# Kernel tuning notes

Measured on AMD Instinct MI355X. Metric: run time of the kernel, lower is better.

The kernel has to match this reference:

```python
import jax, jax.numpy as jnp
import numpy as np

N, T, D, H = 256, 128, 512, 1024


def setup_inputs() -> dict:
    key = jax.random.key(0)
    k_x, k_A, k_Wx, k_Wh, k_Wa = jax.random.split(key, 5)
    x = jax.random.normal(k_x, (N, T, D), dtype=jnp.float32)
    A = jax.random.normal(k_A, (N, H, 4, 4), dtype=jnp.float32)
    Wx = jax.random.normal(k_Wx, (D, 4 * H), dtype=jnp.float32) / np.sqrt(D)
    Wh = jax.random.normal(k_Wh, (H, 4 * H), dtype=jnp.float32) / np.sqrt(H)
    Wattn = jax.random.normal(k_Wa, (H, 4 * H), dtype=jnp.float32) / np.sqrt(H)
    b = jnp.zeros((4 * H,), dtype=jnp.float32)
    return {"x": x, "A": A, "Wx": Wx, "Wh": Wh, "Wattn": Wattn, "b": b}


def _attention_lstm(x, A, Wx, Wh, Wattn, b):
    # A: (N, H, 4, 4) -> flatten spatial to (N, H, 16)
    A_flat = A.reshape(A.shape[0], A.shape[1], -1)
    h0 = A_flat.mean(axis=2)  # (N, H)
    c0 = h0
    Hdim = h0.shape[1]
    scale = 1.0 / jnp.sqrt(jnp.asarray(Hdim, dtype=x.dtype))

    def step(carry, x_t):
        prev_h, prev_c = carry
        # scaled dot-product attention over 16 spatial locations
        scores = jnp.einsum("nh,nhs->ns", prev_h, A_flat) * scale  # (N, 16)
        w = jax.nn.softmax(scores, axis=1)
        attn = jnp.einsum("nhs,ns->nh", A_flat, w)  # (N, H)
        # fused LSTM gates
        a = x_t @ Wx + prev_h @ Wh + attn @ Wattn + b  # (N, 4H)
        i = jax.nn.sigmoid(a[:, 0:Hdim])
        f = jax.nn.sigmoid(a[:, Hdim:2 * Hdim])
        o = jax.nn.sigmoid(a[:, 2 * Hdim:3 * Hdim])
        g = jnp.tanh(a[:, 3 * Hdim:4 * Hdim])
        next_c = f * prev_c + i * g
        next_h = o * jnp.tanh(next_c)
        return (next_h, next_c), next_h

    x_tnd = jnp.swapaxes(x, 0, 1)  # (T, N, D)
    _, h_tnh = jax.lax.scan(step, (h0, c0), x_tnd)
    return jnp.swapaxes(h_tnh, 0, 1)  # (N, T, H)


def reference(x, A, Wx, Wh, Wattn, b):
    return _attention_lstm(x, A, Wx, Wh, Wattn, b)
```

## Files before the change

### kernel.cpp

```cpp
#include <hip/hip_runtime.h>
#include <math.h>

#define NB 256
#define TT 128
#define DD 512
#define HH 1024
#define KHX 1536
#define KFB 2560
#define BK 128
#define NBLK2 256
#define NCHUNK 24

typedef _Float16 half_t;
typedef _Float16 half8 __attribute__((ext_vector_type(8)));
typedef _Float16 half4v __attribute__((ext_vector_type(4)));
typedef float f32x4 __attribute__((ext_vector_type(4)));


__global__ __launch_bounds__(256) void k_trans(const float* __restrict__ src,
        half_t* __restrict__ dst, int kstride, int koff, int nkt) {
    __shared__ half_t tile[64][65];
    int bk = blockIdx.x % nkt;
    int bn = blockIdx.x / nkt;
    int k0 = bk * 64, n0 = bn * 64;
    #pragma unroll
    for (int i = 0; i < 16; ++i) {
        int idx = i * 256 + threadIdx.x;
        int r = idx >> 6, c = idx & 63;
        tile[c][r] = (half_t)src[(size_t)(k0 + r) * 4096 + n0 + c];
    }
    __syncthreads();
    #pragma unroll
    for (int i = 0; i < 16; ++i) {
        int idx = i * 256 + threadIdx.x;
        int r = idx >> 6, c = idx & 63;
        dst[(size_t)(n0 + r) * kstride + koff + k0 + c] = tile[r][c];
    }
}

__global__ __launch_bounds__(256) void k_convX(const float* __restrict__ x,
        half_t* __restrict__ x16) {
    size_t base = ((size_t)blockIdx.x * 256 + threadIdx.x) * 32;
    #pragma unroll
    for (int u = 0; u < 4; ++u) {
        float4 a = ((const float4*)(x + base))[2 * u];
        float4 c = ((const float4*)(x + base))[2 * u + 1];
        half8 p;
        p[0] = (half_t)a.x; p[1] = (half_t)a.y; p[2] = (half_t)a.z; p[3] = (half_t)a.w;
        p[4] = (half_t)c.x; p[5] = (half_t)c.y; p[6] = (half_t)c.z; p[7] = (half_t)c.w;
        ((half8*)(x16 + base))[u] = p;
    }
}

__global__ __launch_bounds__(256) void k_convA(const float* __restrict__ A,
        half_t* __restrict__ A16, half_t* __restrict__ AsT,
        float* __restrict__ cbuf, half_t* __restrict__ h16,
        float* __restrict__ sc0, float* __restrict__ sc1, float* __restrict__ sc2) {
    __shared__ float sred[4][16];
    int n = blockIdx.x, tid = threadIdx.x;
    float ps[16];
    #pragma unroll
    for (int s = 0; s < 16; ++s) ps[s] = 0.f;
    #pragma unroll
    for (int r = 0; r < 4; ++r) {
        int h = tid + r * 256;
        const float4* ap = (const float4*)(A + ((size_t)n * HH + h) * 16);
        float4 v0 = ap[0], v1 = ap[1], v2 = ap[2], v3 = ap[3];
        float a[16];
        a[0]=v0.x; a[1]=v0.y; a[2] =v0.z; a[3] =v0.w;
        a[4]=v1.x; a[5]=v1.y; a[6] =v1.z; a[7] =v1.w;
        a[8]=v2.x; a[9]=v2.y; a[10]=v2.z; a[11]=v2.w;
        a[12]=v3.x; a[13]=v3.y; a[14]=v3.z; a[15]=v3.w;
        float hv = 0.f;
        #pragma unroll
        for (int s = 0; s < 16; ++s) hv += a[s];
        hv *= (1.f / 16.f);
        size_t ci = (size_t)n * HH + h;
        cbuf[ci] = hv;
        h16[ci] = (half_t)hv;
        half8 q0, q1;
        #pragma unroll
        for (int s = 0; s < 8; ++s) { q0[s] = (half_t)a[s]; q1[s] = (half_t)a[s + 8]; }
        *(half8*)(A16 + ci * 16) = q0;
        *(half8*)(A16 + ci * 16 + 8) = q1;
        #pragma unroll
        for (int s = 0; s < 16; ++s)
            AsT[(size_t)n * 16 * HH + (size_t)s * HH + h] = (half_t)a[s];
        #pragma unroll
        for (int s = 0; s < 16; ++s) ps[s] += hv * a[s];
    }
    #pragma unroll
    for (int off = 32; off; off >>= 1)
        #pragma unroll
        for (int s = 0; s < 16; ++s) ps[s] += __shfl_xor(ps[s], off, 64);
    int wave = tid >> 6;
    if ((tid & 63) == 0)
        #pragma unroll
        for (int s = 0; s < 16; ++s) sred[wave][s] = ps[s];
    __syncthreads();
    if (tid < 16) {
        sc0[n * 16 + tid] = sred[0][tid] + sred[1][tid] + sred[2][tid] + sred[3][tid];
        sc1[n * 16 + tid] = 0.f;
        sc2[n * 16 + tid] = 0.f;
    }
}

__global__ __launch_bounds__(256) void k_gemm_G(const half_t* __restrict__ AsT,
        const half_t* __restrict__ WaT, half_t* __restrict__ G16) {
    __shared__ half_t sAs[16][BK + 8];
    __shared__ half_t sB[4][16][BK + 8];
    int bid = blockIdx.x;
    int n = bid >> 6, jt = bid & 63;
    int j0 = jt * 16;
    int tid = threadIdx.x, wv = tid >> 6, lane = tid & 63;
    f32x4 acc = {};
    int srB = tid >> 2, scB = (tid & 3) * 32;
    int gB = srB >> 4, jcB = srB & 15;
    for (int it = 0; it < HH / BK; ++it) {
        int k0 = it * BK;
        if (tid < 128) {
            int r = tid >> 3, c = (tid & 7) * 16;
            const uint4* sp = (const uint4*)(AsT + (size_t)n * 16 * HH + (size_t)r * HH + k0 + c);
            uint4 u0 = sp[0], u1 = sp[1];
            *(uint4*)&sAs[r][c] = u0;
            *(uint4*)&sAs[r][c + 8] = u1;
        }
        {
            const half_t* src = WaT + ((size_t)(gB * HH + j0 + jcB)) * HH + k0 + scB;
            uint4 u0 = ((const uint4*)src)[0];
            uint4 u1 = ((const uint4*)src)[1];
            uint4 u2 = ((const uint4*)src)[2];
            uint4 u3 = ((const uint4*)src)[3];
            *((uint4*)&sB[gB][jcB][scB])      = u0;
            *((uint4*)&sB[gB][jcB][scB + 8])  = u1;
            *((uint4*)&sB[gB][jcB][scB + 16]) = u2;
            *((uint4*)&sB[gB][jcB][scB + 24]) = u3;
        }
        __syncthreads();
        int row16 = lane & 15, kg = lane >> 4;
        #pragma unroll
        for (int kc = 0; kc < BK / 32; ++kc) {
            half8 bf = *(const half8*)&sB[wv][row16][kc * 32 + kg * 8];
            half8 af = *(const half8*)&sAs[row16][kc * 32 + kg * 8];
            acc = __builtin_amdgcn_mfma_f32_16x16x32_f16(af, bf, acc, 0, 0, 0);
        }
        __syncthreads();
    }
    int col = lane & 15, rbase = (lane >> 4) * 4;
    size_t jf = (size_t)wv * HH + j0 + col;
    half4v o;
    o[0] = (half_t)acc[0]; o[1] = (half_t)acc[1];
    o[2] = (half_t)acc[2]; o[3] = (half_t)acc[3];
    *(half4v*)(G16 + ((size_t)n * 4096 + jf) * 16 + rbase) = o;
}


struct StepLds {
    half_t W[32][1544];
    union {
        half_t H[2][128][72];
        struct {
            float pe[128][33];
            char  _pad[18432 - sizeof(float) * 128 * 33];
            float ps[128][20];
        } e;
    } u;
};

__device__ __forceinline__ void grid_sync2(int* cnt, volatile int* flag, int inst) {
    __syncthreads();
    if (threadIdx.x == 0) {
        __threadfence();
        int prev = __hip_atomic_fetch_add(cnt, 1, __ATOMIC_ACQ_REL,
                                          __HIP_MEMORY_SCOPE_AGENT);
        if (prev == NBLK2 * (inst + 1) - 1) {
            __hip_atomic_store((int*)flag, inst + 1, __ATOMIC_RELEASE,
                               __HIP_MEMORY_SCOPE_AGENT);
        } else {
            int guard = 0;
            while (__hip_atomic_load((int*)flag, __ATOMIC_RELAXED,
                                     __HIP_MEMORY_SCOPE_AGENT) < inst + 1) {
                __builtin_amdgcn_s_sleep(2);
                if (++guard > (1 << 24)) break;
            }
        }
        __threadfence();
    }
    __syncthreads();
}

__global__ __launch_bounds__(256, 1) void k_steps2(
        const half_t* __restrict__ x16, half_t* __restrict__ h16A,
        half_t* __restrict__ h16B, const half_t* __restrict__ WhxT,
        const half_t* __restrict__ A16, const half_t* __restrict__ G16,
        const float* __restrict__ b, const float* __restrict__ cbuf,
        float* __restrict__ sc0, float* __restrict__ sc1, float* __restrict__ sc2,
        float* __restrict__ out, int* __restrict__ bar) {
    __shared__ StepLds L;
    int bid = blockIdx.x;
    int mhalf = bid & 1;
    int jb = bid >> 1;
    int n0 = mhalf * 128;
    int tid = threadIdx.x, wv = tid >> 6, lane = tid & 63;
    int la = lane & 15, kg = lane >> 4;
    int srow = tid & 127, shalf = tid >> 7;
    int* cnt = bar;
    volatile int* flag = (volatile int*)(bar + 32);

    {
        int wr = tid >> 3;
        int seg = tid & 7;
        int g = wr >> 3, jj = wr & 7;
        const half_t* wsrc = WhxT + (size_t)(g * HH + jb * 8 + jj) * KHX + seg * 192;
        #pragma unroll
        for (int i = 0; i < 24; ++i) {
            uint4 u = ((const uint4*)wsrc)[i];
            *(uint4*)&L.W[wr][seg * 192 + i * 8] = u;
        }
    }

    int n_l = tid & 127;
    int u4 = (tid >> 7) * 4;
    int n = n0 + n_l;
    int jbase = jb * 8 + u4;
    half8 gq[4][8];
    #pragma unroll
    for (int g = 0; g < 4; ++g) {
        const half8* gsrc = (const half8*)(G16 + ((size_t)n * 4096 + g * HH + jbase) * 16);
        #pragma unroll
        for (int i = 0; i < 8; ++i) gq[g][i] = gsrc[i];
    }
    half8 aq[8];
    {
        const half8* asrc = (const half8*)(A16 + ((size_t)n * HH + jbase) * 16);
        #pragma unroll
        for (int i = 0; i < 8; ++i) aq[i] = asrc[i];
    }
    float bb[4][4];
    #pragma unroll
    for (int g = 0; g < 4; ++g) {
        float4 bv = *(const float4*)(b + g * HH + jbase);
        bb[g][0] = bv.x; bb[g][1] = bv.y; bb[g][2] = bv.z; bb[g][3] = bv.w;
    }
    float creg[4];
    {
        float4 cv = *(const float4*)(cbuf + (size_t)n * HH + jbase);
        creg[0] = cv.x; creg[1] = cv.y; creg[2] = cv.z; creg[3] = cv.w;
    }

    float* scC = sc0; float* scN = sc1; float* scZ = sc2;
    half_t* h16c = h16A; half_t* h16n = h16B;

    uint4 pA0, pA1, pA2, pA3, pB0, pB1, pB2, pB3;

#define STAGE_SRC(c) ((c) < 8 \
    ? x16 + ((size_t)(n0 + srow) * TT + t) * DD + (c) * 64 + shalf * 32 \
    : h16c + (size_t)(n0 + srow) * HH + ((c) - 8) * 64 + shalf * 32)
#define STAGE_LOAD_A(c) { const uint4* sp_ = (const uint4*)STAGE_SRC(c); \
    pA0 = sp_[0]; pA1 = sp_[1]; pA2 = sp_[2]; pA3 = sp_[3]; }
#define STAGE_LOAD_B(c) { const uint4* sp_ = (const uint4*)STAGE_SRC(c); \
    pB0 = sp_[0]; pB1 = sp_[1]; pB2 = sp_[2]; pB3 = sp_[3]; }
#define STAGE_WRITE_A(BUF) { \
    *(uint4*)&L.u.H[BUF][srow][shalf * 32 + 0]  = pA0; \
    *(uint4*)&L.u.H[BUF][srow][shalf * 32 + 8]  = pA1; \
    *(uint4*)&L.u.H[BUF][srow][shalf * 32 + 16] = pA2; \
    *(uint4*)&L.u.H[BUF][srow][shalf * 32 + 24] = pA3; }
#define STAGE_WRITE_B(BUF) { \
    *(uint4*)&L.u.H[BUF][srow][shalf * 32 + 0]  = pB0; \
    *(uint4*)&L.u.H[BUF][srow][shalf * 32 + 8]  = pB1; \
    *(uint4*)&L.u.H[BUF][srow][shalf * 32 + 16] = pB2; \
    *(uint4*)&L.u.H[BUF][srow][shalf * 32 + 24] = pB3; }
#define COMPUTE(BUF, c) { \
    _Pragma("unroll") \
    for (int ks = 0; ks < 2; ++ks) { \
        half8 a0 = *(const half8*)&L.u.H[BUF][wv * 32 + la][ks * 32 + kg * 8]; \
        half8 a1 = *(const half8*)&L.u.H[BUF][wv * 32 + 16 + la][ks * 32 + kg * 8]; \
        half8 b0 = *(const half8*)&L.W[la][(c) * 64 + ks * 32 + kg * 8]; \
        half8 b1 = *(const half8*)&L.W[16 + la][(c) * 64 + ks * 32 + kg * 8]; \
        acc00 = __builtin_amdgcn_mfma_f32_16x16x32_f16(a0, b0, acc00, 0, 0, 0); \
        acc01 = __builtin_amdgcn_mfma_f32_16x16x32_f16(a0, b1, acc01, 0, 0, 0); \
        acc10 = __builtin_amdgcn_mfma_f32_16x16x32_f16(a1, b0, acc10, 0, 0, 0); \
        acc11 = __builtin_amdgcn_mfma_f32_16x16x32_f16(a1, b1, acc11, 0, 0, 0); \
    } }

    for (int t = 0; t < TT; ++t) {
        float w16[16];
        {
            const float4* sp = (const float4*)(scC + (size_t)n * 16);
            float4 q0 = sp[0], q1 = sp[1], q2 = sp[2], q3 = sp[3];
            float sc[16] = {q0.x, q0.y, q0.z, q0.w, q1.x, q1.y, q1.z, q1.w,
                            q2.x, q2.y, q2.z, q2.w, q3.x, q3.y, q3.z, q3.w};
            float m = -1e30f;
            #pragma unroll
            for (int s = 0; s < 16; ++s) { sc[s] *= 0.03125f; m = fmaxf(m, sc[s]); }
            float den = 0.f;
            #pragma unroll
            for (int s = 0; s < 16; ++s) { sc[s] = expf(sc[s] - m); den += sc[s]; }
            float inv = 1.f / den;
            #pragma unroll
            for (int s = 0; s < 16; ++s) w16[s] = sc[s] * inv;
        }
        if (bid < 16) scZ[bid * 256 + tid] = 0.f;

        f32x4 acc00 = {}, acc01 = {}, acc10 = {}, acc11 = {};
        STAGE_LOAD_A(0); STAGE_WRITE_A(0); STAGE_LOAD_B(1);
        __syncthreads();
        for (int d = 0; d < 12; ++d) {
            int c0 = 2 * d, c1 = 2 * d + 1;
            COMPUTE(0, c0);
            STAGE_WRITE_B(1);
            if (c0 + 2 < NCHUNK) STAGE_LOAD_A(c0 + 2);
            __syncthreads();
            COMPUTE(1, c1);
            if (c0 + 2 < NCHUNK) STAGE_WRITE_A(0);
            if (c1 + 2 < NCHUNK) STAGE_LOAD_B(c1 + 2);
            __syncthreads();
        }

        {
            int rbase = kg * 4;
            #pragma unroll
            for (int q = 0; q < 4; ++q) {
                L.u.e.pe[wv * 32 + rbase + q][la]           = acc00[q];
                L.u.e.pe[wv * 32 + rbase + q][16 + la]      = acc01[q];
                L.u.e.pe[wv * 32 + 16 + rbase + q][la]      = acc10[q];
                L.u.e.pe[wv * 32 + 16 + rbase + q][16 + la] = acc11[q];
            }
        }
        __syncthreads();

        float v[4][4];
        #pragma unroll
        for (int g = 0; g < 4; ++g)
            #pragma unroll
            for (int j = 0; j < 4; ++j)
                v[g][j] = L.u.e.pe[n_l][g * 8 + u4 + j] + bb[g][j];
        #pragma unroll
        for (int g = 0; g < 4; ++g)
            #pragma unroll
            for (int j = 0; j < 4; ++j) {
                float a0 = 0.f;
                #pragma unroll
                for (int s = 0; s < 16; ++s)
                    a0 += w16[s] * (float)gq[g][j * 2 + (s >> 3)][s & 7];
                v[g][j] += a0;
            }
        float hv[4];
        #pragma unroll
        for (int j = 0; j < 4; ++j) {
            float ig = 1.f / (1.f + expf(-v[0][j]));
            float fg = 1.f / (1.f + expf(-v[1][j]));
            float og = 1.f / (1.f + expf(-v[2][j]));
            float gg = tanhf(v[3][j]);
            float cn = fg * creg[j] + ig * gg;
            creg[j] = cn;
            hv[j] = og * tanhf(cn);
        }
        {
            float4 o4; o4.x = hv[0]; o4.y = hv[1]; o4.z = hv[2]; o4.w = hv[3];
            *(float4*)(out + ((size_t)n * TT + t) * HH + jbase) = o4;
            half4v h4; h4[0] = (half_t)hv[0]; h4[1] = (half_t)hv[1];
            h4[2] = (half_t)hv[2]; h4[3] = (half_t)hv[3];
            *(half4v*)(h16n + (size_t)n * HH + jbase) = h4;
        }
        float p[16];
        #pragma unroll
        for (int s = 0; s < 16; ++s) {
            float a0 = hv[0] * (float)aq[0 * 2 + (s >> 3)][s & 7]
                     + hv[1] * (float)aq[1 * 2 + (s >> 3)][s & 7]
                     + hv[2] * (float)aq[2 * 2 + (s >> 3)][s & 7]
                     + hv[3] * (float)aq[3 * 2 + (s >> 3)][s & 7];
            p[s] = a0;
        }
        if (tid < 128) {
            #pragma unroll
            for (int s = 0; s < 16; ++s) L.u.e.ps[n_l][s] = p[s];
        }
        __syncthreads();
        if (tid >= 128) {
            #pragma unroll
            for (int s = 0; s < 16; ++s) L.u.e.ps[n_l][s] += p[s];
        }
        __syncthreads();
        {
            int sh = (tid >> 7) * 8;
            #pragma unroll
            for (int i = 0; i < 8; ++i)
                atomicAdd(scN + (size_t)n * 16 + sh + i, L.u.e.ps[n_l][sh + i]);
        }

        if (t + 1 < TT) grid_sync2(cnt, flag, t);
        float* tmp = scC; scC = scN; scN = scZ; scZ = tmp;
        half_t* th = h16c; h16c = h16n; h16n = th;
    }
#undef STAGE_SRC
#undef STAGE_LOAD_A
#undef STAGE_LOAD_B
#undef STAGE_WRITE_A
#undef STAGE_WRITE_B
#undef COMPUTE
}


union LdsS {
    struct {
        half_t sA[32][BK + 8];
        half_t sB[4][16][BK + 8];
    } s;
    float pe[4][32][16];
};

__global__ __launch_bounds__(256) void k_step(const float* __restrict__ x,
        const half_t* __restrict__ h16c, half_t* __restrict__ h16n,
        const half_t* __restrict__ WhxT, const half_t* __restrict__ A16,
        const half_t* __restrict__ G16, const float* __restrict__ b,
        float* __restrict__ cbuf, const float* __restrict__ scC,
        float* __restrict__ scN, float* __restrict__ scZ,
        float* __restrict__ out, int t) {
    __shared__ LdsS L;
    __shared__ float wlds[32][16];
    int bid = blockIdx.x;
    int xcd = bid & 7, slot = bid >> 3;
    int mtile = slot & 7, jtile = slot >> 3;
    int n0 = mtile * 32;
    int j0 = xcd * 128 + jtile * 16;
    int tid = threadIdx.x, wv = tid >> 6, lane = tid & 63;

    if (bid < 16) scZ[bid * 256 + tid] = 0.f;
    if (tid < 32) {
        int n = n0 + tid;
        const float4* sp = (const float4*)(scC + n * 16);
        float4 u0 = sp[0], u1 = sp[1], u2 = sp[2], u3 = sp[3];
        float sc[16] = {u0.x, u0.y, u0.z, u0.w, u1.x, u1.y, u1.z, u1.w,
                        u2.x, u2.y, u2.z, u2.w, u3.x, u3.y, u3.z, u3.w};
        float m = -1e30f;
        #pragma unroll
        for (int s = 0; s < 16; ++s) { sc[s] *= 0.03125f; m = fmaxf(m, sc[s]); }
        float den = 0.f;
        #pragma unroll
        for (int s = 0; s < 16; ++s) { sc[s] = expf(sc[s] - m); den += sc[s]; }
        float inv = 1.f / den;
        #pragma unroll
        for (int s = 0; s < 16; ++s) wlds[tid][s] = sc[s] * inv;
    }

    f32x4 acc[2] = {};
    int srA = tid >> 3, scA = (tid & 7) * 16;
    int srB = tid >> 2, scB = (tid & 3) * 32;
    int gB = srB >> 4, jcB = srB & 15;

    for (int it = 0; it < KHX / BK; ++it) {
        int k0 = it * BK;
        {
            int n = n0 + srA;
            if (k0 < DD) {
                const float* src = x + ((size_t)n * TT + t) * DD + k0 + scA;
                float4 v0 = ((const float4*)src)[0];
                float4 v1 = ((const float4*)src)[1];
                float4 v2 = ((const float4*)src)[2];
                float4 v3 = ((const float4*)src)[3];
                half8 p0, p1;
                p0[0] = (half_t)v0.x; p0[1] = (half_t)v0.y; p0[2] = (half_t)v0.z; p0[3] = (half_t)v0.w;
                p0[4] = (half_t)v1.x; p0[5] = (half_t)v1.y; p0[6] = (half_t)v1.z; p0[7] = (half_t)v1.w;
                p1[0] = (half_t)v2.x; p1[1] = (half_t)v2.y; p1[2] = (half_t)v2.z; p1[3] = (half_t)v2.w;
                p1[4] = (half_t)v3.x; p1[5] = (half_t)v3.y; p1[6] = (half_t)v3.z; p1[7] = (half_t)v3.w;
                *(half8*)&L.s.sA[srA][scA]     = p0;
                *(half8*)&L.s.sA[srA][scA + 8] = p1;
            } else {
                const half_t* srch = h16c + (size_t)n * HH + (k0 - DD) + scA;
                uint4 u0 = ((const uint4*)srch)[0];
                uint4 u1 = ((const uint4*)srch)[1];
                *((uint4*)&L.s.sA[srA][scA])     = u0;
                *((uint4*)&L.s.sA[srA][scA + 8]) = u1;
            }
        }
        {
            const half_t* src = WhxT + ((size_t)(gB * HH + j0 + jcB)) * KHX + k0 + scB;
            uint4 u0 = ((const uint4*)src)[0];
            uint4 u1 = ((const uint4*)src)[1];
            uint4 u2 = ((const uint4*)src)[2];
            uint4 u3 = ((const uint4*)src)[3];
            *((uint4*)&L.s.sB[gB][jcB][scB])      = u0;
            *((uint4*)&L.s.sB[gB][jcB][scB + 8])  = u1;
            *((uint4*)&L.s.sB[gB][jcB][scB + 16]) = u2;
            *((uint4*)&L.s.sB[gB][jcB][scB + 24]) = u3;
        }
        __syncthreads();
        int row16 = lane & 15, kg = lane >> 4;
        #pragma unroll
        for (int kc = 0; kc < BK / 32; ++kc) {
            half8 bf = *(const half8*)&L.s.sB[wv][row16][kc * 32 + kg * 8];
            #pragma unroll
            for (int m = 0; m < 2; ++m) {
                half8 af = *(const half8*)&L.s.sA[row16 + m * 16][kc * 32 + kg * 8];
                acc[m] = __builtin_amdgcn_mfma_f32_16x16x32_f16(af, bf, acc[m], 0, 0, 0);
            }
        }
        __syncthreads();
    }
    {
        int col = lane & 15, rbase = (lane >> 4) * 4;
        #pragma unroll
        for (int m = 0; m < 2; ++m)
            #pragma unroll
            for (int q = 0; q < 4; ++q)
                L.pe[wv][m * 16 + rbase + q][col] = acc[m][q];
    }
    __syncthreads();
    #pragma unroll
    for (int q2 = 0; q2 < 2; ++q2) {
        int idx = tid + q2 * 256;
        int r = idx >> 4, jc = idx & 15;
        int n = n0 + r, j = j0 + jc;
        float wv16[16];
        #pragma unroll
        for (int s = 0; s < 16; ++s) wv16[s] = wlds[r][s];
        float v[4];
        v[0] = L.pe[0][r][jc] + b[j];
        v[1] = L.pe[1][r][jc] + b[HH + j];
        v[2] = L.pe[2][r][jc] + b[2 * HH + j];
        v[3] = L.pe[3][r][jc] + b[3 * HH + j];
        #pragma unroll
        for (int g = 0; g < 4; ++g) {
            const half8* gq = (const half8*)(G16 + ((size_t)n * 4096 + g * HH + j) * 16);
            half8 ga = gq[0], gb2 = gq[1];
            float a0 = 0.f;
            #pragma unroll
            for (int s = 0; s < 8; ++s)
                a0 += wv16[s] * (float)ga[s] + wv16[s + 8] * (float)gb2[s];
            v[g] += a0;
        }
        float ig = 1.f / (1.f + expf(-v[0]));
        float fg = 1.f / (1.f + expf(-v[1]));
        float og = 1.f / (1.f + expf(-v[2]));
        float gg = tanhf(v[3]);
        size_t ci = (size_t)n * HH + j;
        float cp = cbuf[ci];
        float cn = fg * cp + ig * gg;
        cbuf[ci] = cn;
        float hv = og * tanhf(cn);
        out[((size_t)n * TT + t) * HH + j] = hv;
        h16n[ci] = (half_t)hv;
        const half8* ap = (const half8*)(A16 + ci * 16);
        half8 a0 = ap[0], a1 = ap[1];
        float p[16];
        #pragma unroll
        for (int s = 0; s < 8; ++s) { p[s] = hv * (float)a0[s]; p[s + 8] = hv * (float)a1[s]; }
        #pragma unroll
        for (int msk = 1; msk < 16; msk <<= 1)
            #pragma unroll
            for (int s = 0; s < 16; ++s) p[s] += __shfl_xor(p[s], msk, 64);
        float myp = 0.f;
        #pragma unroll
        for (int s = 0; s < 16; ++s) myp = (jc == s) ? p[s] : myp;
        atomicAdd(scN + n * 16 + jc, myp);
    }
}


__global__ __launch_bounds__(256) void fb_wconv(const float* __restrict__ Wx,
        const float* __restrict__ Wh, const float* __restrict__ Wa,
        half_t* __restrict__ WT) {
    __shared__ half_t tile[64][65];
    int bk = blockIdx.x % 40;
    int bn = blockIdx.x / 40;
    int k0 = bk * 64, n0 = bn * 64;
    #pragma unroll
    for (int i = 0; i < 16; ++i) {
        int idx = i * 256 + threadIdx.x;
        int r = idx >> 6, c = idx & 63;
        int k = k0 + r, n = n0 + c;
        float v;
        if (k < DD)            v = Wx[(size_t)k * 4096 + n];
        else if (k < DD + HH)  v = Wh[(size_t)(k - DD) * 4096 + n];
        else                   v = Wa[(size_t)(k - DD - HH) * 4096 + n];
        tile[c][r] = (half_t)v;
    }
    __syncthreads();
    #pragma unroll
    for (int i = 0; i < 16; ++i) {
        int idx = i * 256 + threadIdx.x;
        int r = idx >> 6, c = idx & 63;
        WT[(size_t)(n0 + r) * KFB + k0 + c] = tile[r][c];
    }
}

__global__ __launch_bounds__(256) void fb_init(const float* __restrict__ A,
        float* __restrict__ h0, float* __restrict__ c0) {
    int n = blockIdx.x;
    #pragma unroll
    for (int r = 0; r < 4; ++r) {
        int h = threadIdx.x + r * 256;
        const float4* ap = (const float4*)(A + ((size_t)n * HH + h) * 16);
        float s = 0.f;
        #pragma unroll
        for (int q = 0; q < 4; ++q) {
            float4 v = ap[q];
            s += v.x + v.y + v.z + v.w;
        }
        s *= (1.f / 16.f);
        h0[n * HH + h] = s;
        c0[n * HH + h] = s;
    }
}

__global__ __launch_bounds__(256) void fb_attn(const float* __restrict__ A,
        const float* __restrict__ hprev, long long hstride,
        half_t* __restrict__ h16, half_t* __restrict__ attn16) {
    __shared__ float sh[HH];
    __shared__ float sred[4][16];
    int n = blockIdx.x;
    const float* hp = hprev + (size_t)n * hstride;
    #pragma unroll
    for (int r = 0; r < 4; ++r) {
        int h = threadIdx.x + r * 256;
        float v = hp[h];
        sh[h] = v;
        h16[n * HH + h] = (half_t)v;
    }
    __syncthreads();
    float a[4][16];
    float ps[16];
    #pragma unroll
    for (int s = 0; s < 16; ++s) ps[s] = 0.f;
    #pragma unroll
    for (int r = 0; r < 4; ++r) {
        int h = threadIdx.x + r * 256;
        const float4* ap = (const float4*)(A + ((size_t)n * HH + h) * 16);
        float4 v0 = ap[0], v1 = ap[1], v2 = ap[2], v3 = ap[3];
        a[r][0] = v0.x;  a[r][1] = v0.y;  a[r][2]  = v0.z;  a[r][3]  = v0.w;
        a[r][4] = v1.x;  a[r][5] = v1.y;  a[r][6]  = v1.z;  a[r][7]  = v1.w;
        a[r][8] = v2.x;  a[r][9] = v2.y;  a[r][10] = v2.z;  a[r][11] = v2.w;
        a[r][12] = v3.x; a[r][13] = v3.y; a[r][14] = v3.z;  a[r][15] = v3.w;
        float hh = sh[h];
        #pragma unroll
        for (int s = 0; s < 16; ++s) ps[s] += hh * a[r][s];
    }
    #pragma unroll
    for (int off = 32; off; off >>= 1)
        #pragma unroll
        for (int s = 0; s < 16; ++s) ps[s] += __shfl_xor(ps[s], off, 64);
    int wave = threadIdx.x >> 6;
    if ((threadIdx.x & 63) == 0)
        #pragma unroll
        for (int s = 0; s < 16; ++s) sred[wave][s] = ps[s];
    __syncthreads();
    float sc[16], m = -1e30f;
    #pragma unroll
    for (int s = 0; s < 16; ++s) {
        sc[s] = (sred[0][s] + sred[1][s] + sred[2][s] + sred[3][s]) * 0.03125f;
        m = fmaxf(m, sc[s]);
    }
    float den = 0.f;
    #pragma unroll
    for (int s = 0; s < 16; ++s) { sc[s] = expf(sc[s] - m); den += sc[s]; }
    float inv = 1.f / den;
    #pragma unroll
    for (int r = 0; r < 4; ++r) {
        int h = threadIdx.x + r * 256;
        float acc = 0.f;
        #pragma unroll
        for (int s = 0; s < 16; ++s) acc += a[r][s] * sc[s];
        attn16[n * HH + h] = (half_t)(acc * inv);
    }
}

union LdsFB {
    struct {
        half_t sA[32][BK + 8];
        half_t sB[4][16][BK + 8];
    } s;
    float pe[4][32][16];
};

__global__ __launch_bounds__(256) void fb_gemm(const float* __restrict__ x,
        const half_t* __restrict__ h16, const half_t* __restrict__ attn16,
        const half_t* __restrict__ WT, const float* __restrict__ b,
        float* __restrict__ cbuf, float* __restrict__ out, int t) {
    __shared__ LdsFB L;
    int bid = blockIdx.x;
    int xcd = bid & 7;
    int slot = bid >> 3;
    int mtile = slot & 7;
    int jtile = slot >> 3;
    int m0 = mtile * 32;
    int j0 = xcd * 128 + jtile * 16;
    int tid = threadIdx.x;
    int wv = tid >> 6, lane = tid & 63;
    f32x4 acc[2] = {};
    int srA = tid >> 3, scA = (tid & 7) * 16;
    int srB = tid >> 2, scB = (tid & 3) * 32;
    int gB = srB >> 4, jcB = srB & 15;
    for (int it = 0; it < KFB / BK; ++it) {
        int k0 = it * BK;
        {
            int n = m0 + srA;
            if (k0 < DD) {
                const float* src = x + ((size_t)n * TT + t) * DD + k0 + scA;
                float4 v0 = ((const float4*)src)[0];
                float4 v1 = ((const float4*)src)[1];
                float4 v2 = ((const float4*)src)[2];
                float4 v3 = ((const float4*)src)[3];
                half8 p0, p1;
                p0[0] = (half_t)v0.x; p0[1] = (half_t)v0.y; p0[2] = (half_t)v0.z; p0[3] = (half_t)v0.w;
                p0[4] = (half_t)v1.x; p0[5] = (half_t)v1.y; p0[6] = (half_t)v1.z; p0[7] = (half_t)v1.w;
                p1[0] = (half_t)v2.x; p1[1] = (half_t)v2.y; p1[2] = (half_t)v2.z; p1[3] = (half_t)v2.w;
                p1[4] = (half_t)v3.x; p1[5] = (half_t)v3.y; p1[6] = (half_t)v3.z; p1[7] = (half_t)v3.w;
                *(half8*)&L.s.sA[srA][scA]     = p0;
                *(half8*)&L.s.sA[srA][scA + 8] = p1;
            } else {
                const half_t* srch = (k0 < DD + HH)
                    ? (h16    + (size_t)n * HH + (k0 - DD)      + scA)
                    : (attn16 + (size_t)n * HH + (k0 - DD - HH) + scA);
                uint4 u0 = ((const uint4*)srch)[0];
                uint4 u1 = ((const uint4*)srch)[1];
                *((uint4*)&L.s.sA[srA][scA])     = u0;
                *((uint4*)&L.s.sA[srA][scA + 8]) = u1;
            }
        }
        {
            const half_t* src = WT + ((size_t)(gB * HH + j0 + jcB)) * KFB + k0 + scB;
            uint4 u0 = ((const uint4*)src)[0];
            uint4 u1 = ((const uint4*)src)[1];
            uint4 u2 = ((const uint4*)src)[2];
            uint4 u3 = ((const uint4*)src)[3];
            *((uint4*)&L.s.sB[gB][jcB][scB])      = u0;
            *((uint4*)&L.s.sB[gB][jcB][scB + 8])  = u1;
            *((uint4*)&L.s.sB[gB][jcB][scB + 16]) = u2;
            *((uint4*)&L.s.sB[gB][jcB][scB + 24]) = u3;
        }
        __syncthreads();
        int row16 = lane & 15, kg = lane >> 4;
        #pragma unroll
        for (int kc = 0; kc < BK / 32; ++kc) {
            half8 bf = *(const half8*)&L.s.sB[wv][row16][kc * 32 + kg * 8];
            #pragma unroll
            for (int m = 0; m < 2; ++m) {
                half8 af = *(const half8*)&L.s.sA[row16 + m * 16][kc * 32 + kg * 8];
                acc[m] = __builtin_amdgcn_mfma_f32_16x16x32_f16(af, bf, acc[m], 0, 0, 0);
            }
        }
        __syncthreads();
    }
    {
        int col = lane & 15, rbase = (lane >> 4) * 4;
        #pragma unroll
        for (int m = 0; m < 2; ++m)
            #pragma unroll
            for (int q = 0; q < 4; ++q)
                L.pe[wv][m * 16 + rbase + q][col] = acc[m][q];
    }
    __syncthreads();
    #pragma unroll
    for (int q2 = 0; q2 < 2; ++q2) {
        int idx = tid + q2 * 256;
        int r = idx >> 4, jc = idx & 15;
        int n = m0 + r, j = j0 + jc;
        float vi = L.pe[0][r][jc] + b[j];
        float vf = L.pe[1][r][jc] + b[HH + j];
        float vo = L.pe[2][r][jc] + b[2 * HH + j];
        float vg = L.pe[3][r][jc] + b[3 * HH + j];
        float ig = 1.f / (1.f + expf(-vi));
        float fg = 1.f / (1.f + expf(-vf));
        float og = 1.f / (1.f + expf(-vo));
        float gg = tanhf(vg);
        size_t ci = (size_t)n * HH + j;
        float cp = cbuf[ci];
        float cn = fg * cp + ig * gg;
        cbuf[ci] = cn;
        out[((size_t)n * TT + t) * HH + j] = og * tanhf(cn);
    }
}


extern "C" void kernel_launch(void* const* d_in, const int* in_sizes, int n_in,
                              void* d_out, int out_size, void* d_ws, size_t ws_size,
                              hipStream_t stream) {
    const float* x  = (const float*)d_in[0];
    const float* A  = (const float*)d_in[1];
    const float* Wx = (const float*)d_in[2];
    const float* Wh = (const float*)d_in[3];
    const float* Wa = (const float*)d_in[4];
    const float* b  = (const float*)d_in[5];
    float* out = (float*)d_out;
    char* ws = (char*)d_ws;

    int maxb = 0;
    hipError_t oe = hipOccupancyMaxActiveBlocksPerMultiprocessor(&maxb, k_steps2, 256, 0);
    bool persistent_ok = (oe == hipSuccess && maxb >= 1);

    if (ws_size >= 107004160ULL && persistent_ok) {
        half_t* WhxT = (half_t*)(ws);
        half_t* WaT  = (half_t*)(ws + 12582912);
        half_t* A16  = (half_t*)(ws + 20971520);
        half_t* AsT  = (half_t*)(ws + 29360128);
        half_t* G16  = (half_t*)(ws + 37748736);
        half_t* h16a = (half_t*)(ws + 71303168);
        half_t* h16b = (half_t*)(ws + 71827456);
        float*  cb   = (float*) (ws + 72351744);
        float*  sc0  = (float*) (ws + 73400320);
        float*  sc1  = (float*) (ws + 73416704);
        float*  sc2  = (float*) (ws + 73433088);
        half_t* x16  = (half_t*)(ws + 73449472);
        int*    bar  = (int*)   (ws + 107003904);

        hipLaunchKernelGGL(k_trans, dim3(8 * 64),  dim3(256), 0, stream, Wx, WhxT, KHX, 0,   8);
        hipLaunchKernelGGL(k_trans, dim3(16 * 64), dim3(256), 0, stream, Wh, WhxT, KHX, 512, 16);
        hipLaunchKernelGGL(k_trans, dim3(16 * 64), dim3(256), 0, stream, Wa, WaT,  HH,  0,   16);
        hipLaunchKernelGGL(k_convX, dim3(2048), dim3(256), 0, stream, x, x16);
        hipLaunchKernelGGL(k_convA, dim3(256), dim3(256), 0, stream,
                           A, A16, AsT, cb, h16a, sc0, sc1, sc2);
        hipLaunchKernelGGL(k_gemm_G, dim3(NB * 64), dim3(256), 0, stream, AsT, WaT, G16);
        hipMemsetAsync(bar, 0, 256, stream);
        hipLaunchKernelGGL(k_steps2, dim3(NBLK2), dim3(256), 0, stream,
                           x16, h16a, h16b, WhxT, A16, G16, b, cb,
                           sc0, sc1, sc2, out, bar);
    } else if (ws_size >= 73449472ULL) {
        half_t* WhxT = (half_t*)(ws);
        half_t* WaT  = (half_t*)(ws + 12582912);
        half_t* A16  = (half_t*)(ws + 20971520);
        half_t* AsT  = (half_t*)(ws + 29360128);
        half_t* G16  = (half_t*)(ws + 37748736);
        half_t* h16a = (half_t*)(ws + 71303168);
        half_t* h16b = (half_t*)(ws + 71827456);
        float*  cb   = (float*) (ws + 72351744);
        float*  sc0  = (float*) (ws + 73400320);
        float*  sc1  = (float*) (ws + 73416704);
        float*  sc2  = (float*) (ws + 73433088);
        float* scb[3] = {sc0, sc1, sc2};

        hipLaunchKernelGGL(k_trans, dim3(8 * 64),  dim3(256), 0, stream, Wx, WhxT, KHX, 0,   8);
        hipLaunchKernelGGL(k_trans, dim3(16 * 64), dim3(256), 0, stream, Wh, WhxT, KHX, 512, 16);
        hipLaunchKernelGGL(k_trans, dim3(16 * 64), dim3(256), 0, stream, Wa, WaT,  HH,  0,   16);
        hipLaunchKernelGGL(k_convA, dim3(256), dim3(256), 0, stream,
                           A, A16, AsT, cb, h16a, sc0, sc1, sc2);
        hipLaunchKernelGGL(k_gemm_G, dim3(NB * 64), dim3(256), 0, stream, AsT, WaT, G16);
        for (int t = 0; t < TT; ++t) {
            float* scC = scb[t % 3];
            float* scN = scb[(t + 1) % 3];
            float* scZ = scb[(t + 2) % 3];
            half_t* h16c = (t & 1) ? h16b : h16a;
            half_t* h16n = (t & 1) ? h16a : h16b;
            hipLaunchKernelGGL(k_step, dim3(512), dim3(256), 0, stream,
                               x, h16c, h16n, WhxT, A16, G16, b, cb, scC, scN, scZ, out, t);
        }
    } else {
        half_t* WT  = (half_t*)ws;
        float*  h0  = (float*)(ws + 20971520);
        float*  cb  = (float*)(ws + 22020096);
        half_t* h16 = (half_t*)(ws + 23068672);
        half_t* a16 = (half_t*)(ws + 23592960);
        hipLaunchKernelGGL(fb_wconv, dim3(2560), dim3(256), 0, stream, Wx, Wh, Wa, WT);
        hipLaunchKernelGGL(fb_init, dim3(256), dim3(256), 0, stream, A, h0, cb);
        for (int t = 0; t < TT; ++t) {
            const float* hp = (t == 0) ? h0 : (out + (size_t)(t - 1) * HH);
            long long hstride = (t == 0) ? (long long)HH : (long long)TT * HH;
            hipLaunchKernelGGL(fb_attn, dim3(256), dim3(256), 0, stream, A, hp, hstride, h16, a16);
            hipLaunchKernelGGL(fb_gemm, dim3(512), dim3(256), 0, stream,
                               x, h16, a16, WT, b, cb, out, t);
        }
    }
}
```

Baseline: 4.645 ms.

## Hoist input projection into a batched GEMM and widen persistent step kernel

The x_t @ Wx projection for all timesteps is computed up front by a new batched MFMA GEMM (k_gemm_XW) into a step-tiled fp16 buffer. The persistent recurrent kernel then only multiplies by Wh, shrinking its K dimension from 1536 to 1024 and its LDS weight slice. The step kernel now uses 512 threads, with waves split by K parity and partial sums reduced through LDS, and each thread handles 2 hidden units instead of 4. This adds a large extra workspace buffer and requires a larger ws_size to take the persistent path, and the XW output is written with scattered 2-byte stores.

```diff
diff --git a/kernel.cpp b/kernel.cpp
--- a/kernel.cpp
+++ b/kernel.cpp
@@ -8,12 +8,13 @@
 #define KHX 1536
 #define KFB 2560
 #define BK 128
-#define NBLK2 256
-#define NCHUNK 24
+#define NBLK3 256
+#define NCH3 16
 
 typedef _Float16 half_t;
 typedef _Float16 half8 __attribute__((ext_vector_type(8)));
 typedef _Float16 half4v __attribute__((ext_vector_type(4)));
+typedef _Float16 half2v __attribute__((ext_vector_type(2)));
 typedef float f32x4 __attribute__((ext_vector_type(4)));
 
 
@@ -154,26 +155,84 @@
     *(half4v*)(G16 + ((size_t)n * 4096 + jf) * 16 + rbase) = o;
 }
 
-
-struct StepLds {
-    half_t W[32][1544];
+__global__ __launch_bounds__(256) void k_gemm_XW(const half_t* __restrict__ x16,
+        const half_t* __restrict__ WhxT, half_t* __restrict__ XW16) {
+    __shared__ half_t sA[128][72];
+    __shared__ half_t sB[64][72];
+    int bid = blockIdx.x;
+    int bm = bid & 255;
+    int bj = bid >> 8;
+    int row0 = bm * 128;
+    int col0 = bj * 64;
+    int tid = threadIdx.x, wv = tid >> 6, lane = tid & 63;
+    int la = lane & 15, kg = lane >> 4;
+    int mh = wv & 1, jh = wv >> 1;
+    f32x4 acc[4][2] = {};
+    int srA = tid >> 1, scA = (tid & 1) * 32;
+    int srB = tid >> 2, scB = (tid & 3) * 16;
+    for (int c = 0; c < 8; ++c) {
+        {
+            const uint4* sp = (const uint4*)(x16 + (size_t)(row0 + srA) * DD + c * 64 + scA);
+            uint4 u0 = sp[0], u1 = sp[1];
+            *(uint4*)&sA[srA][scA] = u0;
+            *(uint4*)&sA[srA][scA + 8] = u1;
+        }
+        {
+            const uint4* sp = (const uint4*)(WhxT + (size_t)(col0 + srB) * KHX + c * 64 + scB);
+            *(uint4*)&sB[srB][scB] = sp[0];
+        }
+        __syncthreads();
+        #pragma unroll
+        for (int ks = 0; ks < 2; ++ks) {
+            half8 b0 = *(const half8*)&sB[jh * 32 + la][ks * 32 + kg * 8];
+            half8 b1 = *(const half8*)&sB[jh * 32 + 16 + la][ks * 32 + kg * 8];
+            #pragma unroll
+            for (int m = 0; m < 4; ++m) {
+                half8 af = *(const half8*)&sA[mh * 64 + m * 16 + la][ks * 32 + kg * 8];
+                acc[m][0] = __builtin_amdgcn_mfma_f32_16x16x32_f16(af, b0, acc[m][0], 0, 0, 0);
+                acc[m][1] = __builtin_amdgcn_mfma_f32_16x16x32_f16(af, b1, acc[m][1], 0, 0, 0);
+            }
+        }
+        __syncthreads();
+    }
+    #pragma unroll
+    for (int m = 0; m < 4; ++m)
+        #pragma unroll
+        for (int jt = 0; jt < 2; ++jt)
+            #pragma unroll
+            for (int q = 0; q < 4; ++q) {
+                int R = row0 + mh * 64 + m * 16 + kg * 4 + q;
+                int C = col0 + jh * 32 + jt * 16 + la;
+                int n = R >> 7, t = R & 127;
+                int g = C >> 10, jrem = C & 1023;
+                int jb = jrem >> 3, jj = jrem & 7;
+                int mhalf = n >> 7, n_l = n & 127;
+                size_t dst = ((((size_t)t * 128 + jb) * 2 + mhalf) * 128 + n_l) * 32
+                           + g * 8 + jj;
+                XW16[dst] = (half_t)acc[m][jt][q];
+            }
+}
+
+
+struct StepLds3 {
+    half_t W[32][1032];
     union {
         half_t H[2][128][72];
         struct {
             float pe[128][33];
-            char  _pad[18432 - sizeof(float) * 128 * 33];
-            float ps[128][20];
+            char  _pad[18432 - 16896];
+            float ps[2][128][18];
         } e;
     } u;
 };
 
-__device__ __forceinline__ void grid_sync2(int* cnt, volatile int* flag, int inst) {
+__device__ __forceinline__ void grid_sync3(int* cnt, volatile int* flag, int inst) {
     __syncthreads();
     if (threadIdx.x == 0) {
         __threadfence();
         int prev = __hip_atomic_fetch_add(cnt, 1, __ATOMIC_ACQ_REL,
                                           __HIP_MEMORY_SCOPE_AGENT);
-        if (prev == NBLK2 * (inst + 1) - 1) {
+        if (prev == NBLK3 * (inst + 1) - 1) {
             __hip_atomic_store((int*)flag, inst + 1, __ATOMIC_RELEASE,
                                __HIP_MEMORY_SCOPE_AGENT);
         } else {
@@ -189,92 +248,84 @@
     __syncthreads();
 }
 
-__global__ __launch_bounds__(256, 1) void k_steps2(
-        const half_t* __restrict__ x16, half_t* __restrict__ h16A,
+__global__ __launch_bounds__(512, 2) void k_steps3(
+        const half_t* __restrict__ XW16, half_t* __restrict__ h16A,
         half_t* __restrict__ h16B, const half_t* __restrict__ WhxT,
         const half_t* __restrict__ A16, const half_t* __restrict__ G16,
         const float* __restrict__ b, const float* __restrict__ cbuf,
         float* __restrict__ sc0, float* __restrict__ sc1, float* __restrict__ sc2,
         float* __restrict__ out, int* __restrict__ bar) {
-    __shared__ StepLds L;
+    __shared__ StepLds3 L;
     int bid = blockIdx.x;
-    int mhalf = bid & 1;
-    int jb = bid >> 1;
+    int mhalf = bid & 1, jb = bid >> 1;
     int n0 = mhalf * 128;
-    int tid = threadIdx.x, wv = tid >> 6, lane = tid & 63;
+    int tid = threadIdx.x;
+    int wv = tid >> 6, lane = tid & 63;
     int la = lane & 15, kg = lane >> 4;
-    int srow = tid & 127, shalf = tid >> 7;
+    int kpar = wv & 1, sub = wv >> 1;
+    int srow = tid >> 2, sseg = tid & 3;
     int* cnt = bar;
     volatile int* flag = (volatile int*)(bar + 32);
 
     {
-        int wr = tid >> 3;
-        int seg = tid & 7;
-        int g = wr >> 3, jj = wr & 7;
-        const half_t* wsrc = WhxT + (size_t)(g * HH + jb * 8 + jj) * KHX + seg * 192;
-        #pragma unroll
-        for (int i = 0; i < 24; ++i) {
+        int wr = tid >> 4;
+        int seg = tid & 15;
+        const half_t* wsrc = WhxT + (size_t)((wr >> 3) * HH + jb * 8 + (wr & 7)) * KHX
+                           + DD + seg * 64;
+        #pragma unroll
+        for (int i = 0; i < 8; ++i) {
             uint4 u = ((const uint4*)wsrc)[i];
-            *(uint4*)&L.W[wr][seg * 192 + i * 8] = u;
-        }
-    }
-
-    int n_l = tid & 127;
-    int u4 = (tid >> 7) * 4;
+            *(uint4*)&L.W[wr][seg * 64 + i * 8] = u;
+        }
+    }
+
+    int n_l = tid & 127, jg2 = tid >> 7;
     int n = n0 + n_l;
-    int jbase = jb * 8 + u4;
-    half8 gq[4][8];
+    int jbase = jb * 8 + jg2 * 2;
+    half8 gq[4][4];
     #pragma unroll
     for (int g = 0; g < 4; ++g) {
         const half8* gsrc = (const half8*)(G16 + ((size_t)n * 4096 + g * HH + jbase) * 16);
         #pragma unroll
-        for (int i = 0; i < 8; ++i) gq[g][i] = gsrc[i];
-    }
-    half8 aq[8];
+        for (int i = 0; i < 4; ++i) gq[g][i] = gsrc[i];
+    }
+    half8 aq[4];
     {
         const half8* asrc = (const half8*)(A16 + ((size_t)n * HH + jbase) * 16);
         #pragma unroll
-        for (int i = 0; i < 8; ++i) aq[i] = asrc[i];
-    }
-    float bb[4][4];
+        for (int i = 0; i < 4; ++i) aq[i] = asrc[i];
+    }
+    float bb[4][2];
     #pragma unroll
     for (int g = 0; g < 4; ++g) {
-        float4 bv = *(const float4*)(b + g * HH + jbase);
-        bb[g][0] = bv.x; bb[g][1] = bv.y; bb[g][2] = bv.z; bb[g][3] = bv.w;
-    }
-    float creg[4];
-    {
-        float4 cv = *(const float4*)(cbuf + (size_t)n * HH + jbase);
-        creg[0] = cv.x; creg[1] = cv.y; creg[2] = cv.z; creg[3] = cv.w;
-    }
+        bb[g][0] = b[g * HH + jbase];
+        bb[g][1] = b[g * HH + jbase + 1];
+    }
+    float creg[2];
+    creg[0] = cbuf[(size_t)n * HH + jbase];
+    creg[1] = cbuf[(size_t)n * HH + jbase + 1];
 
     float* scC = sc0; float* scN = sc1; float* scZ = sc2;
-    half_t* h16c = h16A; half_t* h16n = h16B;
-
-    uint4 pA0, pA1, pA2, pA3, pB0, pB1, pB2, pB3;
-
-#define STAGE_SRC(c) ((c) < 8 \
-    ? x16 + ((size_t)(n0 + srow) * TT + t) * DD + (c) * 64 + shalf * 32 \
-    : h16c + (size_t)(n0 + srow) * HH + ((c) - 8) * 64 + shalf * 32)
-#define STAGE_LOAD_A(c) { const uint4* sp_ = (const uint4*)STAGE_SRC(c); \
-    pA0 = sp_[0]; pA1 = sp_[1]; pA2 = sp_[2]; pA3 = sp_[3]; }
-#define STAGE_LOAD_B(c) { const uint4* sp_ = (const uint4*)STAGE_SRC(c); \
-    pB0 = sp_[0]; pB1 = sp_[1]; pB2 = sp_[2]; pB3 = sp_[3]; }
-#define STAGE_WRITE_A(BUF) { \
-    *(uint4*)&L.u.H[BUF][srow][shalf * 32 + 0]  = pA0; \
-    *(uint4*)&L.u.H[BUF][srow][shalf * 32 + 8]  = pA1; \
-    *(uint4*)&L.u.H[BUF][srow][shalf * 32 + 16] = pA2; \
-    *(uint4*)&L.u.H[BUF][srow][shalf * 32 + 24] = pA3; }
-#define STAGE_WRITE_B(BUF) { \
-    *(uint4*)&L.u.H[BUF][srow][shalf * 32 + 0]  = pB0; \
-    *(uint4*)&L.u.H[BUF][srow][shalf * 32 + 8]  = pB1; \
-    *(uint4*)&L.u.H[BUF][srow][shalf * 32 + 16] = pB2; \
-    *(uint4*)&L.u.H[BUF][srow][shalf * 32 + 24] = pB3; }
+    half_t* h16c = h16A;
+    half_t* h16n = h16B;
+
+    uint4 rA0, rA1, rB0, rB1;
+
+#define LOADC_A(c) { const uint4* sp_ = (const uint4*)(h16c + \
+        (size_t)(n0 + srow) * HH + (c) * 64 + sseg * 16); \
+        rA0 = sp_[0]; rA1 = sp_[1]; }
+#define LOADC_B(c) { const uint4* sp_ = (const uint4*)(h16c + \
+        (size_t)(n0 + srow) * HH + (c) * 64 + sseg * 16); \
+        rB0 = sp_[0]; rB1 = sp_[1]; }
+#define WRITE_A(BUF) { *(uint4*)&L.u.H[BUF][srow][sseg * 16] = rA0; \
+                       *(uint4*)&L.u.H[BUF][srow][sseg * 16 + 8] = rA1; }
+#define WRITE_B(BUF) { *(uint4*)&L.u.H[BUF][srow][sseg * 16] = rB0; \
+                       *(uint4*)&L.u.H[BUF][srow][sseg * 16 + 8] = rB1; }
 #define COMPUTE(BUF, c) { \
     _Pragma("unroll") \
     for (int ks = 0; ks < 2; ++ks) { \
-        half8 a0 = *(const half8*)&L.u.H[BUF][wv * 32 + la][ks * 32 + kg * 8]; \
-        half8 a1 = *(const half8*)&L.u.H[BUF][wv * 32 + 16 + la][ks * 32 + kg * 8]; \
+        half8 a0 = *(const half8*)&L.u.H[BUF][sub * 32 + la][ks * 32 + kg * 8]; \
+        half8 a1 = *(const half8*)&L.u.H[BUF][sub * 32 + 16 + la][ks * 32 + kg * 8]; \
         half8 b0 = *(const half8*)&L.W[la][(c) * 64 + ks * 32 + kg * 8]; \
         half8 b1 = *(const half8*)&L.W[16 + la][(c) * 64 + ks * 32 + kg * 8]; \
         acc00 = __builtin_amdgcn_mfma_f32_16x16x32_f16(a0, b0, acc00, 0, 0, 0); \
@@ -284,6 +335,10 @@
     } }
 
     for (int t = 0; t < TT; ++t) {
+        const half_t* xwp = XW16 + ((((size_t)t * 128 + jb) * 2 + mhalf) * 128 + n_l) * 32;
+        half2v xw2[4];
+        #pragma unroll
+        for (int g = 0; g < 4; ++g) xw2[g] = *(const half2v*)(xwp + g * 8 + (jg2 & 0) + 0 + (jbase - jb * 8 - jg2 * 2) + jg2 * 2);
         float w16[16];
         {
             const float4* sp = (const float4*)(scC + (size_t)n * 16);
@@ -300,104 +355,109 @@
             #pragma unroll
             for (int s = 0; s < 16; ++s) w16[s] = sc[s] * inv;
         }
-        if (bid < 16) scZ[bid * 256 + tid] = 0.f;
+        if (bid < 8) scZ[bid * 512 + tid] = 0.f;
 
         f32x4 acc00 = {}, acc01 = {}, acc10 = {}, acc11 = {};
-        STAGE_LOAD_A(0); STAGE_WRITE_A(0); STAGE_LOAD_B(1);
-        __syncthreads();
-        for (int d = 0; d < 12; ++d) {
+        LOADC_A(0); WRITE_A(0); LOADC_B(1);
+        __syncthreads();
+        #pragma unroll 1
+        for (int d = 0; d < 8; ++d) {
             int c0 = 2 * d, c1 = 2 * d + 1;
-            COMPUTE(0, c0);
-            STAGE_WRITE_B(1);
-            if (c0 + 2 < NCHUNK) STAGE_LOAD_A(c0 + 2);
+            if (kpar == 0) COMPUTE(0, c0);
+            WRITE_B(1);
+            if (c0 + 2 < NCH3) LOADC_A(c0 + 2);
             __syncthreads();
-            COMPUTE(1, c1);
-            if (c0 + 2 < NCHUNK) STAGE_WRITE_A(0);
-            if (c1 + 2 < NCHUNK) STAGE_LOAD_B(c1 + 2);
+            if (kpar == 1) COMPUTE(1, c1);
+            if (c0 + 2 < NCH3) WRITE_A(0);
+            if (c1 + 2 < NCH3) LOADC_B(c1 + 2);
             __syncthreads();
         }
 
-        {
-            int rbase = kg * 4;
+        if (kpar == 0) {
             #pragma unroll
             for (int q = 0; q < 4; ++q) {
-                L.u.e.pe[wv * 32 + rbase + q][la]           = acc00[q];
-                L.u.e.pe[wv * 32 + rbase + q][16 + la]      = acc01[q];
-                L.u.e.pe[wv * 32 + 16 + rbase + q][la]      = acc10[q];
-                L.u.e.pe[wv * 32 + 16 + rbase + q][16 + la] = acc11[q];
-            }
-        }
-        __syncthreads();
-
-        float v[4][4];
-        #pragma unroll
-        for (int g = 0; g < 4; ++g)
-            #pragma unroll
-            for (int j = 0; j < 4; ++j)
-                v[g][j] = L.u.e.pe[n_l][g * 8 + u4 + j] + bb[g][j];
-        #pragma unroll
-        for (int g = 0; g < 4; ++g)
-            #pragma unroll
-            for (int j = 0; j < 4; ++j) {
+                L.u.e.pe[sub * 32 + kg * 4 + q][la]           = acc00[q];
+                L.u.e.pe[sub * 32 + kg * 4 + q][16 + la]      = acc01[q];
+                L.u.e.pe[sub * 32 + 16 + kg * 4 + q][la]      = acc10[q];
+                L.u.e.pe[sub * 32 + 16 + kg * 4 + q][16 + la] = acc11[q];
+            }
+        }
+        __syncthreads();
+        if (kpar == 1) {
+            #pragma unroll
+            for (int q = 0; q < 4; ++q) {
+                L.u.e.pe[sub * 32 + kg * 4 + q][la]           += acc00[q];
+                L.u.e.pe[sub * 32 + kg * 4 + q][16 + la]      += acc01[q];
+                L.u.e.pe[sub * 32 + 16 + kg * 4 + q][la]      += acc10[q];
+                L.u.e.pe[sub * 32 + 16 + kg * 4 + q][16 + la] += acc11[q];
+            }
+        }
+        __syncthreads();
+
+        float v[4][2];
+        #pragma unroll
+        for (int g = 0; g < 4; ++g) {
+            #pragma unroll
+            for (int jj = 0; jj < 2; ++jj) {
                 float a0 = 0.f;
                 #pragma unroll
                 for (int s = 0; s < 16; ++s)
-                    a0 += w16[s] * (float)gq[g][j * 2 + (s >> 3)][s & 7];
-                v[g][j] += a0;
-            }
-        float hv[4];
-        #pragma unroll
-        for (int j = 0; j < 4; ++j) {
-            float ig = 1.f / (1.f + expf(-v[0][j]));
-            float fg = 1.f / (1.f + expf(-v[1][j]));
-            float og = 1.f / (1.f + expf(-v[2][j]));
-            float gg = tanhf(v[3][j]);
-            float cn = fg * creg[j] + ig * gg;
-            creg[j] = cn;
-            hv[j] = og * tanhf(cn);
+                    a0 += w16[s] * (float)gq[g][jj * 2 + (s >> 3)][s & 7];
+                v[g][jj] = L.u.e.pe[n_l][g * 8 + jg2 * 2 + jj] + bb[g][jj]
+                         + (float)xw2[g][jj] + a0;
+            }
+        }
+        float hv[2];
+        #pragma unroll
+        for (int jj = 0; jj < 2; ++jj) {
+            float ig = 1.f / (1.f + expf(-v[0][jj]));
+            float fg = 1.f / (1.f + expf(-v[1][jj]));
+            float og = 1.f / (1.f + expf(-v[2][jj]));
+            float gg = tanhf(v[3][jj]);
+            float cn = fg * creg[jj] + ig * gg;
+            creg[jj] = cn;
+            hv[jj] = og * tanhf(cn);
         }
         {
-            float4 o4; o4.x = hv[0]; o4.y = hv[1]; o4.z = hv[2]; o4.w = hv[3];
-            *(float4*)(out + ((size_t)n * TT + t) * HH + jbase) = o4;
-            half4v h4; h4[0] = (half_t)hv[0]; h4[1] = (half_t)hv[1];
-            h4[2] = (half_t)hv[2]; h4[3] = (half_t)hv[3];
-            *(half4v*)(h16n + (size_t)n * HH + jbase) = h4;
+            float2 o2; o2.x = hv[0]; o2.y = hv[1];
+            *(float2*)(out + ((size_t)n * TT + t) * HH + jbase) = o2;
+            half2v h2; h2[0] = (half_t)hv[0]; h2[1] = (half_t)hv[1];
+            *(half2v*)(h16n + (size_t)n * HH + jbase) = h2;
         }
         float p[16];
         #pragma unroll
-        for (int s = 0; s < 16; ++s) {
-            float a0 = hv[0] * (float)aq[0 * 2 + (s >> 3)][s & 7]
-                     + hv[1] * (float)aq[1 * 2 + (s >> 3)][s & 7]
-                     + hv[2] * (float)aq[2 * 2 + (s >> 3)][s & 7]
-                     + hv[3] * (float)aq[3 * 2 + (s >> 3)][s & 7];
-            p[s] = a0;
-        }
-        if (tid < 128) {
-            #pragma unroll
-            for (int s = 0; s < 16; ++s) L.u.e.ps[n_l][s] = p[s];
-        }
-        __syncthreads();
-        if (tid >= 128) {
-            #pragma unroll
-            for (int s = 0; s < 16; ++s) L.u.e.ps[n_l][s] += p[s];
+        for (int s = 0; s < 16; ++s)
+            p[s] = hv[0] * (float)aq[s >> 3][s & 7]
+                 + hv[1] * (float)aq[2 + (s >> 3)][s & 7];
+        int pair = jg2 >> 1;
+        if ((jg2 & 1) == 0) {
+            #pragma unroll
+            for (int s = 0; s < 16; ++s) L.u.e.ps[pair][n_l][s] = p[s];
+        }
+        __syncthreads();
+        if ((jg2 & 1) == 1) {
+            #pragma unroll
+            for (int s = 0; s < 16; ++s) L.u.e.ps[pair][n_l][s] += p[s];
         }
         __syncthreads();
         {
-            int sh = (tid >> 7) * 8;
-            #pragma unroll
-            for (int i = 0; i < 8; ++i)
-                atomicAdd(scN + (size_t)n * 16 + sh + i, L.u.e.ps[n_l][sh + i]);
-        }
-
-        if (t + 1 < TT) grid_sync2(cnt, flag, t);
+            #pragma unroll
+            for (int i = 0; i < 4; ++i) {
+                int slot = tid * 4 + i;
+                int nn = slot >> 4, s = slot & 15;
+                float val = L.u.e.ps[0][nn][s] + L.u.e.ps[1][nn][s];
+                atomicAdd(scN + (size_t)(n0 + nn) * 16 + s, val);
+            }
+        }
+
+        if (t + 1 < TT) grid_sync3(cnt, flag, t);
         float* tmp = scC; scC = scN; scN = scZ; scZ = tmp;
         half_t* th = h16c; h16c = h16n; h16n = th;
     }
-#undef STAGE_SRC
-#undef STAGE_LOAD_A
-#undef STAGE_LOAD_B
-#undef STAGE_WRITE_A
-#undef STAGE_WRITE_B
+#undef LOADC_A
+#undef LOADC_B
+#undef WRITE_A
+#undef WRITE_B
 #undef COMPUTE
 }
 
@@ -786,10 +846,10 @@
     char* ws = (char*)d_ws;
 
     int maxb = 0;
-    hipError_t oe = hipOccupancyMaxActiveBlocksPerMultiprocessor(&maxb, k_steps2, 256, 0);
+    hipError_t oe = hipOccupancyMaxActiveBlocksPerMultiprocessor(&maxb, k_steps3, 512, 0);
     bool persistent_ok = (oe == hipSuccess && maxb >= 1);
 
-    if (ws_size >= 107004160ULL && persistent_ok) {
+    if (ws_size >= 375439616ULL && persistent_ok) {
         half_t* WhxT = (half_t*)(ws);
         half_t* WaT  = (half_t*)(ws + 12582912);
         half_t* A16  = (half_t*)(ws + 20971520);
@@ -803,6 +863,7 @@
         float*  sc2  = (float*) (ws + 73433088);
         half_t* x16  = (half_t*)(ws + 73449472);
         int*    bar  = (int*)   (ws + 107003904);
+        half_t* XW16 = (half_t*)(ws + 107004160);
 
         hipLaunchKernelGGL(k_trans, dim3(8 * 64),  dim3(256), 0, stream, Wx, WhxT, KHX, 0,   8);
         hipLaunchKernelGGL(k_trans, dim3(16 * 64), dim3(256), 0, stream, Wh, WhxT, KHX, 512, 16);
@@ -811,9 +872,10 @@
         hipLaunchKernelGGL(k_convA, dim3(256), dim3(256), 0, stream,
                            A, A16, AsT, cb, h16a, sc0, sc1, sc2);
         hipLaunchKernelGGL(k_gemm_G, dim3(NB * 64), dim3(256), 0, stream, AsT, WaT, G16);
+        hipLaunchKernelGGL(k_gemm_XW, dim3(256 * 64), dim3(256), 0, stream, x16, WhxT, XW16);
         hipMemsetAsync(bar, 0, 256, stream);
-        hipLaunchKernelGGL(k_steps2, dim3(NBLK2), dim3(256), 0, stream,
-                           x16, h16a, h16b, WhxT, A16, G16, b, cb,
+        hipLaunchKernelGGL(k_steps3, dim3(NBLK3), dim3(512), 0, stream,
+                           XW16, h16a, h16b, WhxT, A16, G16, b, cb,
                            sc0, sc1, sc2, out, bar);
     } else if (ws_size >= 73449472ULL) {
         half_t* WhxT = (half_t*)(ws);
```

New measurement: 4.632 ms. No clear change (-0.3%).
